# Performance work log

Measured on AMD Instinct MI355X. Metric: run time of the kernel, lower is better.

The kernel has to match this reference:

```python
import jax, jax.numpy as jnp
import numpy as np

OMEGA_0 = 30.0  # SIREN frequency from init_kwargs


def setup_inputs() -> dict:
    key = jax.random.key(0)
    ks = jax.random.split(key, 8)
    B, Cin, Cout, H, L = 64, 64, 64, 128, 8192
    return {
        "x": jax.random.normal(ks[0], (B, Cin, L), dtype=jnp.float32),
        "w1": jax.random.normal(ks[1], (H, 1), dtype=jnp.float32) * (1.0 / 1.0),
        "b1": jax.random.normal(ks[2], (H,), dtype=jnp.float32) * 0.1,
        "w2": jax.random.normal(ks[3], (H, H), dtype=jnp.float32) * (1.0 / np.sqrt(H)),
        "b2": jax.random.normal(ks[4], (H,), dtype=jnp.float32) * 0.1,
        "w3": jax.random.normal(ks[5], (Cout * Cin, H), dtype=jnp.float32) * (1.0 / np.sqrt(H)),
        "b3": jax.random.normal(ks[6], (Cout * Cin,), dtype=jnp.float32) * 0.1,
        "bias": jnp.zeros((Cout,), dtype=jnp.float32),
    }


def reference(x, w1, b1, w2, b2, w3, b3, bias):
    B, Cin, L = x.shape
    Cout = bias.shape[0]
    # 1. relative positions in [-1, 1], one per input timestep
    rel = jnp.linspace(-1.0, 1.0, L)  # [L]
    # 2. SIREN kernel-generating MLP (1x1 convs over positions == per-position MLP)
    h = jnp.sin(OMEGA_0 * (rel[:, None] * w1[:, 0][None, :] + b1))       # [L, H]
    h = jnp.sin(OMEGA_0 * (h @ w2.T + b2))                               # [L, H]
    k = h @ w3.T + b3                                                    # [L, Cout*Cin]
    # torch: Kernel output [1, Cout*Cin, L].view(Cout, Cin, L)
    kernel = k.T.reshape(Cout, Cin, L)                                   # [Cout, Cin, L]
    # 3. conv1d with padding=0 and kernel length == L -> single output position
    #    (cross-correlation, exactly torch.nn.functional.conv1d)
    out = jnp.einsum("bil,oil->bo", x, kernel) + bias                    # [B, Cout]
    return out[:, :, None]                                               # [B, Cout, 1]
```

## Files before the change

### kernel.cpp

```cpp
#include <hip/hip_runtime.h>
#include <hip/hip_bf16.h>

#define LPOS 8192
#define HDIM 128
#define M_TOT 4096
#define GROW  136
#define GELEMS (M_TOT * GROW)
#define KSPLIT 16
#define CUNITS 1024
#define BUNITS (4 * CUNITS)
#define NPART 256

typedef float  f32x4 __attribute__((ext_vector_type(4)));
typedef short  s16x8 __attribute__((ext_vector_type(8)));
typedef unsigned int u32x4 __attribute__((ext_vector_type(4)));

__device__ __forceinline__ unsigned short bf16_rne(float f) {
    unsigned u = __builtin_bit_cast(unsigned, f);
    u += 0x7fffu + ((u >> 16) & 1u);
    return (unsigned short)(u >> 16);
}
__device__ __forceinline__ float bf16f(unsigned short v) {
    return __builtin_bit_cast(float, (unsigned)v << 16);
}

__device__ __forceinline__ s16x8 cvt8(f32x4 a, f32x4 b) {
    s16x8 r;
    r[0] = (short)bf16_rne(a[0]); r[1] = (short)bf16_rne(a[1]);
    r[2] = (short)bf16_rne(a[2]); r[3] = (short)bf16_rne(a[3]);
    r[4] = (short)bf16_rne(b[0]); r[5] = (short)bf16_rne(b[1]);
    r[6] = (short)bf16_rne(b[2]); r[7] = (short)bf16_rne(b[3]);
    return r;
}

__device__ __forceinline__ float sum8(f32x4 a, f32x4 b) {
    return ((a[0] + a[1]) + (a[2] + a[3])) + ((b[0] + b[1]) + (b[2] + b[3]));
}

__global__ __launch_bounds__(256) void k1_siren(
        const float* __restrict__ w1, const float* __restrict__ b1,
        const float* __restrict__ w2, const float* __restrict__ b2,
        unsigned short* __restrict__ h2T) {
    __shared__ float w2sT[HDIM * 129];
    __shared__ __align__(16) float h1s[2][HDIM * 8];
    const int tid = threadIdx.x;
    const int s = tid >> 7;
    const int h = tid & 127;

    for (int idx = tid; idx < HDIM * HDIM; idx += 256)
        w2sT[(idx & 127) * 129 + (idx >> 7)] = w2[idx];

    const int l0 = blockIdx.x * 16 + s * 8;
    const float myw1 = w1[h], myb1 = b1[h];
    #pragma unroll
    for (int ls = 0; ls < 8; ++ls) {
        float rel = -1.0f + (2.0f / 8191.0f) * (float)(l0 + ls);
        h1s[s][h * 8 + ls] = __sinf(30.0f * (rel * myw1 + myb1));
    }
    __syncthreads();

    const float bb = b2[h];
    float acc[8];
    #pragma unroll
    for (int ls = 0; ls < 8; ++ls) acc[ls] = bb;

    for (int j = 0; j < HDIM; ++j) {
        float wv = w2sT[j * 129 + h];
        const f32x4* hp = (const f32x4*)&h1s[s][j * 8];
        f32x4 p0 = hp[0], p1 = hp[1];
        acc[0] += wv * p0[0]; acc[1] += wv * p0[1];
        acc[2] += wv * p0[2]; acc[3] += wv * p0[3];
        acc[4] += wv * p1[0]; acc[5] += wv * p1[1];
        acc[6] += wv * p1[2]; acc[7] += wv * p1[3];
    }

    u32x4 ov;
    #pragma unroll
    for (int q = 0; q < 4; ++q) {
        unsigned lo = bf16_rne(__sinf(30.0f * acc[2 * q]));
        unsigned hi = bf16_rne(__sinf(30.0f * acc[2 * q + 1]));
        ov[q] = lo | (hi << 16);
    }
    const size_t c = (size_t)(l0 >> 6);
    const int k8 = (l0 >> 3) & 7;
    *(u32x4*)(h2T + (c * CUNITS + (size_t)k8 * 128 + h) * 8) = ov;
}

__global__ __launch_bounds__(256, 2) void k2_gemm(
        const float* __restrict__ x, const unsigned short* __restrict__ h2T,
        unsigned short* __restrict__ gp) {
    __shared__ unsigned short lds[BUNITS * 8];

    const int lane = threadIdx.x & 63;
    const int wv   = threadIdx.x >> 6;
    const int r    = lane & 15;
    const int kg   = lane >> 4;
    const int m0   = blockIdx.x * 128;
    const int y8   = blockIdx.y;
    const int kc   = y8 * 512;

    const float* xpa = x + (size_t)(m0 + wv * 32 + r) * LPOS + kc + kg * 8;
    const float* xpb = xpa + 16 * LPOS;

    f32x4 xr[2][2][4];

#define LOADX(SL, IT) do { \
        xr[SL][0][0] = *(const f32x4*)(xpa + (IT) * 64);      \
        xr[SL][0][1] = *(const f32x4*)(xpa + (IT) * 64 + 4);  \
        xr[SL][0][2] = *(const f32x4*)(xpa + (IT) * 64 + 32); \
        xr[SL][0][3] = *(const f32x4*)(xpa + (IT) * 64 + 36); \
        xr[SL][1][0] = *(const f32x4*)(xpb + (IT) * 64);      \
        xr[SL][1][1] = *(const f32x4*)(xpb + (IT) * 64 + 4);  \
        xr[SL][1][2] = *(const f32x4*)(xpb + (IT) * 64 + 32); \
        xr[SL][1][3] = *(const f32x4*)(xpb + (IT) * 64 + 36); \
    } while (0)

    f32x4 acc[2][8];
    #pragma unroll
    for (int s = 0; s < 2; ++s)
        #pragma unroll
        for (int t = 0; t < 8; ++t) { f32x4 z = {0.f,0.f,0.f,0.f}; acc[s][t] = z; }
    float sacc0 = 0.f, sacc1 = 0.f;

    #pragma unroll 1
    for (int g = 0; g < 2; ++g) {
        const int base = g * 4;
        {
            const unsigned short* src = h2T + (size_t)(y8 * 2 + g) * (BUNITS * 8);
            #pragma unroll
            for (int j = 0; j < 16; ++j) {
                const int U = j * 256 + threadIdx.x;
                __builtin_amdgcn_global_load_lds(
                    (const unsigned int*)(src + (size_t)U * 8),
                    (unsigned int*)&lds[U * 8], 16, 0, 0);
            }
        }
        LOADX(0, base); LOADX(1, base + 1);
        __syncthreads();

        #pragma unroll
        for (int it = 0; it < 4; ++it) {
            const int sl = it & 1;
            s16x8 a0lo = cvt8(xr[sl][0][0], xr[sl][0][1]);
            s16x8 a0hi = cvt8(xr[sl][0][2], xr[sl][0][3]);
            s16x8 a1lo = cvt8(xr[sl][1][0], xr[sl][1][1]);
            s16x8 a1hi = cvt8(xr[sl][1][2], xr[sl][1][3]);
            sacc0 += sum8(xr[sl][0][0], xr[sl][0][1]) + sum8(xr[sl][0][2], xr[sl][0][3]);
            sacc1 += sum8(xr[sl][1][0], xr[sl][1][1]) + sum8(xr[sl][1][2], xr[sl][1][3]);
            if (it + 2 < 4) LOADX(sl, base + it + 2);

            #pragma unroll
            for (int t = 0; t < 8; ++t) {
                s16x8 blo = *(const s16x8*)&lds[((size_t)it * CUNITS + kg * 128 + t * 16 + r) * 8];
                s16x8 bhi = *(const s16x8*)&lds[((size_t)it * CUNITS + (kg + 4) * 128 + t * 16 + r) * 8];
                acc[0][t] = __builtin_amdgcn_mfma_f32_16x16x32_bf16(a0lo, blo, acc[0][t], 0, 0, 0);
                acc[0][t] = __builtin_amdgcn_mfma_f32_16x16x32_bf16(a0hi, bhi, acc[0][t], 0, 0, 0);
                acc[1][t] = __builtin_amdgcn_mfma_f32_16x16x32_bf16(a1lo, blo, acc[1][t], 0, 0, 0);
                acc[1][t] = __builtin_amdgcn_mfma_f32_16x16x32_bf16(a1hi, bhi, acc[1][t], 0, 0, 0);
            }
        }
        __syncthreads();
    }
#undef LOADX

    unsigned short* gpy = gp + (size_t)y8 * GELEMS;
    #pragma unroll
    for (int s = 0; s < 2; ++s) {
        #pragma unroll
        for (int t = 0; t < 8; ++t) {
            const int col = t * 16 + r;
            #pragma unroll
            for (int q = 0; q < 4; ++q) {
                const int row = m0 + wv * 32 + s * 16 + kg * 4 + q;
                const int ii = row & 63, bb2 = row >> 6;
                gpy[((size_t)ii * 64 + bb2) * GROW + col] = bf16_rne(acc[s][t][q]);
            }
        }
    }
    sacc0 += __shfl_xor(sacc0, 16); sacc0 += __shfl_xor(sacc0, 32);
    sacc1 += __shfl_xor(sacc1, 16); sacc1 += __shfl_xor(sacc1, 32);
    if (kg == 0) {
        const int rowA = m0 + wv * 32 + r;
        const int rowB = rowA + 16;
        gpy[((size_t)(rowA & 63) * 64 + (rowA >> 6)) * GROW + 128] = bf16_rne(sacc0);
        gpy[((size_t)(rowB & 63) * 64 + (rowB >> 6)) * GROW + 128] = bf16_rne(sacc1);
    }
}

__global__ __launch_bounds__(256, 3) void k3_mm(
        const unsigned short* __restrict__ gp, const float* __restrict__ w3,
        const float* __restrict__ b3, float* __restrict__ part) {
    __shared__ unsigned short As[2][64 * 128];
    __shared__ unsigned short Bs[64 * 128];
    __shared__ float b3s[64];
    __shared__ float sls[64];

    const int bid = blockIdx.x;
    const int i   = bid >> 2;
    const int y0  = (bid & 3) * 4;
    const int t    = threadIdx.x;
    const int lane = t & 63;
    const int w    = t >> 6;
    const int r    = lane & 15;
    const int kg   = lane >> 4;

    #pragma unroll
    for (int p = 0; p < 4; ++p) {
        const int row  = p * 16 + (t >> 4);
        const int gran = t & 15;
        const float* src = w3 + (size_t)(row * 64 + i) * HDIM + gran * 8;
        f32x4 v0 = *(const f32x4*)src;
        f32x4 v1 = *(const f32x4*)(src + 4);
        *(s16x8*)&Bs[row * 128 + ((gran ^ (row & 7)) * 8)] = cvt8(v0, v1);
    }
    if (t < 64) b3s[t] = b3[t * 64 + i];

    float sreg = 0.f;
    auto stageA = [&](int y, int d) {
        const unsigned short* src = gp + (size_t)y * GELEMS + (size_t)i * (64 * GROW);
        #pragma unroll
        for (int p = 0; p < 4; ++p) {
            const int b    = p * 16 + (t >> 4);
            const int gran = t & 15;
            s16x8 v = *(const s16x8*)(src + (size_t)b * GROW + gran * 8);
            *(s16x8*)&As[d][b * 128 + ((gran ^ (b & 7)) * 8)] = v;
        }
        if (t < 64) sreg += bf16f(src[(size_t)t * GROW + 128]);
    };

    stageA(y0, 0);
    __syncthreads();

    s16x8 bfr[4][4];
    #pragma unroll
    for (int ct = 0; ct < 4; ++ct) {
        const int o = ct * 16 + r;
        #pragma unroll
        for (int ks = 0; ks < 4; ++ks)
            bfr[ct][ks] = *(const s16x8*)&Bs[o * 128 + (((ks * 4 + kg) ^ (o & 7)) * 8)];
    }

    f32x4 acc[4];
    #pragma unroll
    for (int ct = 0; ct < 4; ++ct) { f32x4 z = {0.f,0.f,0.f,0.f}; acc[ct] = z; }

    const int bA = w * 16 + r;
    #pragma unroll
    for (int yy = 0; yy < 4; ++yy) {
        if (yy + 1 < 4) stageA(y0 + yy + 1, (yy + 1) & 1);
        const unsigned short* buf = &As[yy & 1][0];
        s16x8 af[4];
        #pragma unroll
        for (int ks = 0; ks < 4; ++ks)
            af[ks] = *(const s16x8*)&buf[bA * 128 + (((ks * 4 + kg) ^ (bA & 7)) * 8)];
        #pragma unroll
        for (int ct = 0; ct < 4; ++ct)
            #pragma unroll
            for (int ks = 0; ks < 4; ++ks)
                acc[ct] = __builtin_amdgcn_mfma_f32_16x16x32_bf16(af[ks], bfr[ct][ks], acc[ct], 0, 0, 0);
        __syncthreads();
    }

    if (t < 64) sls[t] = sreg;
    __syncthreads();

    float* po = part + (size_t)bid * 4096;
    #pragma unroll
    for (int ct = 0; ct < 4; ++ct) {
        const int o = ct * 16 + r;
        #pragma unroll
        for (int q = 0; q < 4; ++q) {
            const int b = w * 16 + kg * 4 + q;
            po[b * 64 + o] = acc[ct][q] + sls[b] * b3s[o];
        }
    }
}

__global__ __launch_bounds__(256) void k4_final(
        const float* __restrict__ part, const float* __restrict__ bias,
        float* __restrict__ out) {
    const int idx = blockIdx.x * 256 + threadIdx.x;
    float s = bias[idx & 63];
    #pragma unroll 8
    for (int p = 0; p < NPART; ++p)
        s += part[(size_t)p * 4096 + idx];
    out[idx] = s;
}

extern "C" void kernel_launch(void* const* d_in, const int* in_sizes, int n_in,
                              void* d_out, int out_size, void* d_ws, size_t ws_size,
                              hipStream_t stream) {
    (void)in_sizes; (void)n_in; (void)out_size; (void)ws_size;
    const float* x    = (const float*)d_in[0];
    const float* w1   = (const float*)d_in[1];
    const float* b1   = (const float*)d_in[2];
    const float* w2   = (const float*)d_in[3];
    const float* b2   = (const float*)d_in[4];
    const float* w3   = (const float*)d_in[5];
    const float* b3   = (const float*)d_in[6];
    const float* bias = (const float*)d_in[7];
    float* out = (float*)d_out;

    char* ws = (char*)d_ws;
    unsigned short* h2T = (unsigned short*)ws;
    const size_t H2T_BYTES = (size_t)(LPOS / 64) * CUNITS * 16;
    unsigned short* gp = (unsigned short*)(ws + H2T_BYTES);
    const size_t GP_BYTES = (size_t)KSPLIT * GELEMS * 2;
    float* part = (float*)(ws + H2T_BYTES + GP_BYTES);

    k1_siren<<<LPOS / 16, 256, 0, stream>>>(w1, b1, w2, b2, h2T);
    k2_gemm<<<dim3(M_TOT / 128, KSPLIT), 256, 0, stream>>>(x, h2T, gp);
    k3_mm<<<NPART, 256, 0, stream>>>(gp, w3, b3, part);
    k4_final<<<16, 256, 0, stream>>>(part, bias, out);
}
```

Baseline: 65.06 us.

## Triple-buffer k3 A tiles with register prefetch and split k4 reduction across waves

k3_mm switches from a two-buffer LDS ring to three buffers. Global loads are issued into registers ahead of time and written to LDS later, so load latency overlaps the MFMA work and fewer barriers are needed. k4_final now launches 64 blocks instead of 16; each block splits the 256 partial sums across four waves and reduces them through shared memory, which adds parallelism to the final reduction. The costs are more LDS and registers per block in k3, the removed occupancy hint, and a different summation order in k4.

```diff
diff --git a/kernel.cpp b/kernel.cpp
--- a/kernel.cpp
+++ b/kernel.cpp
@@ -187,10 +187,10 @@
     }
 }
 
-__global__ __launch_bounds__(256, 3) void k3_mm(
+__global__ __launch_bounds__(256) void k3_mm(
         const unsigned short* __restrict__ gp, const float* __restrict__ w3,
         const float* __restrict__ b3, float* __restrict__ part) {
-    __shared__ unsigned short As[2][64 * 128];
+    __shared__ unsigned short As[3][64 * 128];
     __shared__ unsigned short Bs[64 * 128];
     __shared__ float b3s[64];
     __shared__ float sls[64];
@@ -203,11 +203,12 @@
     const int w    = t >> 6;
     const int r    = lane & 15;
     const int kg   = lane >> 4;
+    const int bbr  = t >> 4;
+    const int gran = t & 15;
 
     #pragma unroll
     for (int p = 0; p < 4; ++p) {
-        const int row  = p * 16 + (t >> 4);
-        const int gran = t & 15;
+        const int row = p * 16 + bbr;
         const float* src = w3 + (size_t)(row * 64 + i) * HDIM + gran * 8;
         f32x4 v0 = *(const f32x4*)src;
         f32x4 v1 = *(const f32x4*)(src + 4);
@@ -216,19 +217,28 @@
     if (t < 64) b3s[t] = b3[t * 64 + i];
 
     float sreg = 0.f;
-    auto stageA = [&](int y, int d) {
-        const unsigned short* src = gp + (size_t)y * GELEMS + (size_t)i * (64 * GROW);
-        #pragma unroll
-        for (int p = 0; p < 4; ++p) {
-            const int b    = p * 16 + (t >> 4);
-            const int gran = t & 15;
-            s16x8 v = *(const s16x8*)(src + (size_t)b * GROW + gran * 8);
-            *(s16x8*)&As[d][b * 128 + ((gran ^ (b & 7)) * 8)] = v;
-        }
-        if (t < 64) sreg += bf16f(src[(size_t)t * GROW + 128]);
-    };
-
-    stageA(y0, 0);
+    const unsigned short* gpi = gp + (size_t)i * (64 * GROW);
+
+    s16x8 va[4]; unsigned short ra = 0;
+    s16x8 vb[4]; unsigned short rb = 0;
+
+#define ISSUE(Y, V, R_) do { \
+        const unsigned short* src_ = gpi + (size_t)(Y) * GELEMS; \
+        _Pragma("unroll") for (int p_ = 0; p_ < 4; ++p_) \
+            V[p_] = *(const s16x8*)(src_ + (size_t)(p_ * 16 + bbr) * GROW + gran * 8); \
+        if (t < 64) R_ = src_[(size_t)t * GROW + 128]; \
+    } while (0)
+
+#define WRITE(D, V, R_) do { \
+        _Pragma("unroll") for (int p_ = 0; p_ < 4; ++p_) { \
+            const int row_ = p_ * 16 + bbr; \
+            *(s16x8*)&As[D][row_ * 128 + ((gran ^ (row_ & 7)) * 8)] = V[p_]; } \
+        if (t < 64) sreg += bf16f(R_); \
+    } while (0)
+
+    ISSUE(y0, va, ra);     WRITE(0, va, ra);
+    ISSUE(y0 + 1, vb, rb); WRITE(1, vb, rb);
+    ISSUE(y0 + 2, va, ra);
     __syncthreads();
 
     s16x8 bfr[4][4];
@@ -245,21 +255,29 @@
     for (int ct = 0; ct < 4; ++ct) { f32x4 z = {0.f,0.f,0.f,0.f}; acc[ct] = z; }
 
     const int bA = w * 16 + r;
-    #pragma unroll
-    for (int yy = 0; yy < 4; ++yy) {
-        if (yy + 1 < 4) stageA(y0 + yy + 1, (yy + 1) & 1);
-        const unsigned short* buf = &As[yy & 1][0];
-        s16x8 af[4];
-        #pragma unroll
-        for (int ks = 0; ks < 4; ++ks)
-            af[ks] = *(const s16x8*)&buf[bA * 128 + (((ks * 4 + kg) ^ (bA & 7)) * 8)];
-        #pragma unroll
-        for (int ct = 0; ct < 4; ++ct)
-            #pragma unroll
-            for (int ks = 0; ks < 4; ++ks)
-                acc[ct] = __builtin_amdgcn_mfma_f32_16x16x32_bf16(af[ks], bfr[ct][ks], acc[ct], 0, 0, 0);
-        __syncthreads();
-    }
+#define COMPUTE(D) do { \
+        const unsigned short* buf_ = &As[D][0]; \
+        s16x8 af_[4]; \
+        _Pragma("unroll") for (int ks = 0; ks < 4; ++ks) \
+            af_[ks] = *(const s16x8*)&buf_[bA * 128 + (((ks * 4 + kg) ^ (bA & 7)) * 8)]; \
+        _Pragma("unroll") for (int ct = 0; ct < 4; ++ct) \
+            _Pragma("unroll") for (int ks = 0; ks < 4; ++ks) \
+                acc[ct] = __builtin_amdgcn_mfma_f32_16x16x32_bf16(af_[ks], bfr[ct][ks], acc[ct], 0, 0, 0); \
+    } while (0)
+
+    COMPUTE(0);
+    WRITE(2, va, ra);
+    ISSUE(y0 + 3, vb, rb);
+    __syncthreads();
+    COMPUTE(1);
+    WRITE(0, vb, rb);
+    __syncthreads();
+    COMPUTE(2);
+    COMPUTE(0);
+
+#undef COMPUTE
+#undef WRITE
+#undef ISSUE
 
     if (t < 64) sls[t] = sreg;
     __syncthreads();
@@ -279,12 +297,20 @@
 __global__ __launch_bounds__(256) void k4_final(
         const float* __restrict__ part, const float* __restrict__ bias,
         float* __restrict__ out) {
-    const int idx = blockIdx.x * 256 + threadIdx.x;
-    float s = bias[idx & 63];
+    __shared__ float red[4][64];
+    const int t  = threadIdx.x;
+    const int il = t & 63;
+    const int pg = t >> 6;
+    const int idx = blockIdx.x * 64 + il;
+
+    float s = 0.f;
     #pragma unroll 8
-    for (int p = 0; p < NPART; ++p)
+    for (int p = pg * 64; p < pg * 64 + 64; ++p)
         s += part[(size_t)p * 4096 + idx];
-    out[idx] = s;
+    red[pg][il] = s;
+    __syncthreads();
+    if (t < 64)
+        out[blockIdx.x * 64 + t] = bias[t] + ((red[0][t] + red[1][t]) + (red[2][t] + red[3][t]));
 }
 
 extern "C" void kernel_launch(void* const* d_in, const int* in_sizes, int n_in,
@@ -311,5 +337,5 @@
     k1_siren<<<LPOS / 16, 256, 0, stream>>>(w1, b1, w2, b2, h2T);
     k2_gemm<<<dim3(M_TOT / 128, KSPLIT), 256, 0, stream>>>(x, h2T, gp);
     k3_mm<<<NPART, 256, 0, stream>>>(gp, w3, b3, part);
-    k4_final<<<16, 256, 0, stream>>>(part, bias, out);
-}
+    k4_final<<<64, 256, 0, stream>>>(part, bias, out);
+}
```

New measurement: 62.00 us. -4.7%, faster.
